# Optimization experiments

Measured on AMD Instinct MI355X. Metric: run time of the kernel, lower is better.

The kernel has to match this reference:

```python
import jax, jax.numpy as jnp
import numpy as np

N_NODES = 100000
N_EDGES = 1000000
D_FEAT = 64
THR_LO, THR_HI = 0.6, 0.8
LOG_CLAMP = -100.0  # torch BCELoss clamps log terms at -100


def setup_inputs() -> dict:
    key = jax.random.key(0)
    k1, k2, k3 = jax.random.split(key, 3)
    edges_nn = jax.random.randint(k1, (N_EDGES, 2), 0, N_NODES, dtype=jnp.int64)
    probas = jax.random.uniform(k2, (N_NODES,), dtype=jnp.float32)
    feats = jax.random.normal(k3, (N_NODES, D_FEAT), dtype=jnp.float32)
    return {"edges_nn": edges_nn, "probas": probas, "feats": feats}


def reference(edges_nn, probas, feats):
    # Per-edge endpoint probabilities. [E]
    pi = probas[edges_nn[:, 0]]
    pj = probas[edges_nn[:, 1]]

    # Similar edges: both endpoints confidently positive (label 1).
    mask_sim = (pi >= THR_HI) & (pj >= THR_HI)
    # Dissimilar edges: one confident positive, the other confident negative (label 0).
    mask_disim = ((pi >= THR_HI) & (pj < THR_LO)) | ((pj >= THR_HI) & (pi < THR_LO))

    # Gather endpoint features and compute pairwise L2 distance for ALL edges
    # (masked afterwards; avoids dynamic shapes, stays jit-friendly). [E, D] -> [E]
    diff = feats[edges_nn[:, 0]] - feats[edges_nn[:, 1]]
    d = jnp.sqrt(jnp.sum(diff * diff, axis=1))
    p = jnp.exp(-d)  # predicted similarity in (0, 1]

    # BCE per edge (torch-style log clamping at -100).
    #   sim   (target 1): -log(p)   = d (clamped)
    #   disim (target 0): -log(1-p)
    bce_sim = -jnp.maximum(jnp.log(p), LOG_CLAMP)
    bce_disim = -jnp.maximum(jnp.log1p(-p), LOG_CLAMP)

    n_sim = jnp.sum(mask_sim).astype(jnp.float32)
    n_disim = jnp.sum(mask_disim).astype(jnp.float32)
    total = n_sim + n_disim

    # Class-balancing weights from the original: sim edges weighted by the
    # fraction of disim edges and vice versa.
    pos_weight = n_disim / total
    neg_weight = n_sim / total

    sim_sum = jnp.sum(jnp.where(mask_sim, bce_sim, 0.0))
    disim_sum = jnp.sum(jnp.where(mask_disim, bce_disim, 0.0))

    loss = (sim_sum * pos_weight + disim_sum * neg_weight) / total
    return loss
```

## Files before the change

### kernel.cpp

```cpp
#include <hip/hip_runtime.h>
#include <math.h>

#define N_EDGES   1000000
#define N_NODES   100000
#define THR_LO    0.6f
#define THR_HI    0.8f
#define LOG_CLAMP -100.0f

#define NBLOCKS   2048
#define BLOCK     256

#define CLS_OFF   0x8000
#define QF_OFF    0x10000

#if defined(__has_builtin)
#if __has_builtin(__builtin_amdgcn_cvt_pk_fp8_f32) && __has_builtin(__builtin_amdgcn_cvt_pk_f32_fp8)
#define HAVE_FP8_CVT 1
#endif
#endif

typedef float v2f __attribute__((ext_vector_type(2)));

__device__ __forceinline__ unsigned f32_to_fp8_sw(float f) {
    unsigned u = __float_as_uint(f);
    unsigned s = (u >> 24) & 0x80u;
    float a = fabsf(f);
    if (a >= 448.f) return s | 0x7Eu;
    unsigned au = u & 0x7FFFFFFFu;
    int E = (int)(au >> 23) - 127;
    if (E >= -6) {
        unsigned m   = au & 0x7FFFFFu;
        unsigned keep = m >> 20;
        unsigned rem  = m & 0xFFFFFu;
        keep += (rem > 0x80000u) || (rem == 0x80000u && (keep & 1u));
        unsigned val = (((unsigned)(E + 7)) << 3) + keep;
        return s | val;
    } else {
        float q = a * 512.0f;
        unsigned k = (unsigned)(q + 0.5f);
        return s | k;
    }
}

__device__ __forceinline__ unsigned pack4_fp8(float4 v) {
#if HAVE_FP8_CVT
    int w = 0;
    w = __builtin_amdgcn_cvt_pk_fp8_f32(v.x, v.y, w, false);
    w = __builtin_amdgcn_cvt_pk_fp8_f32(v.z, v.w, w, true);
    return (unsigned)w;
#else
    return f32_to_fp8_sw(v.x) | (f32_to_fp8_sw(v.y) << 8) |
           (f32_to_fp8_sw(v.z) << 16) | (f32_to_fp8_sw(v.w) << 24);
#endif
}

__device__ __forceinline__ float fp8_to_f32_sw(unsigned byte) {
    unsigned s  = (byte & 0x80u) << 24;
    unsigned em = (byte & 0x7Fu) << 20;
    return __uint_as_float(s | em) * 0x1p+120f;
}

__device__ __forceinline__ float sq8(unsigned a, unsigned b) {
#if HAVE_FP8_CVT
    v2f a0 = __builtin_amdgcn_cvt_pk_f32_fp8((int)a, false);
    v2f a1 = __builtin_amdgcn_cvt_pk_f32_fp8((int)a, true);
    v2f b0 = __builtin_amdgcn_cvt_pk_f32_fp8((int)b, false);
    v2f b1 = __builtin_amdgcn_cvt_pk_f32_fp8((int)b, true);
    float d0 = a0.x - b0.x, d1 = a0.y - b0.y;
    float d2 = a1.x - b1.x, d3 = a1.y - b1.y;
#else
    float d0 = fp8_to_f32_sw(a & 255u)         - fp8_to_f32_sw(b & 255u);
    float d1 = fp8_to_f32_sw((a >> 8) & 255u)  - fp8_to_f32_sw((b >> 8) & 255u);
    float d2 = fp8_to_f32_sw((a >> 16) & 255u) - fp8_to_f32_sw((b >> 16) & 255u);
    float d3 = fp8_to_f32_sw(a >> 24)          - fp8_to_f32_sw(b >> 24);
#endif
    return d0 * d0 + d1 * d1 + d2 * d2 + d3 * d3;
}

__device__ __forceinline__ float sq16(uint4 A, uint4 B) {
    return sq8(A.x, B.x) + sq8(A.y, B.y) + sq8(A.z, B.z) + sq8(A.w, B.w);
}

__device__ __forceinline__ void accum_edge(float s, int simflag,
                                           float& sim, float& dis) {
    float d = sqrtf(s);
    if (simflag) {
        sim += fminf(d, 100.0f);
    } else {
        float p = expf(-d);
        dis += -fmaxf(log1pf(-p), LOG_CLAMP);
    }
}

__global__ void __launch_bounds__(BLOCK)
prep_kernel(const float* __restrict__ probas,
            const float4* __restrict__ feats,
            unsigned* __restrict__ cls,
            unsigned* __restrict__ qf) {
    int t = blockIdx.x * blockDim.x + threadIdx.x;
    const int NF4 = N_NODES * 16;
    if (t < NF4) {
        qf[t] = pack4_fp8(feats[t]);
    }
    if (t < N_NODES / 16) {
        unsigned w = 0;
        #pragma unroll
        for (int k = 0; k < 16; ++k) {
            float p = probas[t * 16 + k];
            unsigned c = (p >= THR_HI ? 1u : 0u) | (p < THR_LO ? 2u : 0u);
            w |= c << (2 * k);
        }
        cls[t] = w;
    }
}

__global__ void __launch_bounds__(BLOCK)
edge_loss_kernel(const int2* __restrict__ edges,
                 const unsigned* __restrict__ cls,
                 const uint4* __restrict__ qfeat,
                 float4* __restrict__ part) {
    const int lane = threadIdx.x & 63;
    const int wave = threadIdx.x >> 6;
    const int grp  = lane >> 2;
    const int sub  = lane & 3;

    __shared__ int sh_i[4][64];
    __shared__ int sh_j[4][64];

    float sim = 0.f, dis = 0.f, ns = 0.f, nd = 0.f;

    const int gstride = gridDim.x * blockDim.x;
    for (int base = blockIdx.x * blockDim.x; base < N_EDGES; base += gstride) {
        int e = base + threadIdx.x;
        bool in = (e < N_EDGES);
        int2 ij = in ? edges[e] : make_int2(0, 0);
        unsigned ci = (cls[ij.x >> 4] >> ((ij.x & 15) * 2)) & 3u;
        unsigned cj = (cls[ij.y >> 4] >> ((ij.y & 15) * 2)) & 3u;
        bool msim = in && ((ci & cj & 1u) != 0u);
        bool mdis = in && ((((ci & 1u) & (cj >> 1)) | ((cj & 1u) & (ci >> 1))) != 0u);

        unsigned long long balsim = __ballot(msim);
        unsigned long long baldis = __ballot(mdis);
        unsigned long long m      = balsim | baldis;
        if (lane == 0) {
            ns += (float)__popcll(balsim);
            nd += (float)__popcll(baldis);
        }
        int count = __popcll(m);

        if (msim | mdis) {
            int prefix = __popcll(m & ((1ULL << lane) - 1ULL));
            sh_i[wave][prefix] = ij.x | (msim ? (int)0x80000000 : 0);
            sh_j[wave][prefix] = ij.y;
        }
        __syncthreads();

        for (int t = grp; t < count; t += 32) {
            bool h2 = (t + 16) < count;
            int  tb = h2 ? t + 16 : t;

            int xa_i = sh_i[wave][t],  xa_j = sh_j[wave][t];
            int xb_i = sh_i[wave][tb], xb_j = sh_j[wave][tb];

            const uint4* rai = qfeat + (size_t)(xa_i & 0x7FFFFFFF) * 4;
            const uint4* raj = qfeat + (size_t)xa_j * 4;
            const uint4* rbi = qfeat + (size_t)(xb_i & 0x7FFFFFFF) * 4;
            const uint4* rbj = qfeat + (size_t)xb_j * 4;

            uint4 A = rai[sub];
            uint4 B = raj[sub];
            uint4 C = rbi[sub];
            uint4 D = rbj[sub];

            float s1 = sq16(A, B);
            float s2 = sq16(C, D);

            s1 += __shfl_xor(s1, 1); s1 += __shfl_xor(s1, 2);
            s2 += __shfl_xor(s2, 1); s2 += __shfl_xor(s2, 2);

            if (sub == 0) {
                accum_edge(s1, ((unsigned)xa_i) >> 31, sim, dis);
                if (h2) accum_edge(s2, ((unsigned)xb_i) >> 31, sim, dis);
            }
        }
        __syncthreads();
    }

    #pragma unroll
    for (int off = 32; off > 0; off >>= 1) {
        sim += __shfl_down(sim, off);
        dis += __shfl_down(dis, off);
        ns  += __shfl_down(ns,  off);
        nd  += __shfl_down(nd,  off);
    }
    __shared__ float lds[4][4];
    if (lane == 0) {
        lds[wave][0] = sim; lds[wave][1] = dis;
        lds[wave][2] = ns;  lds[wave][3] = nd;
    }
    __syncthreads();
    if (threadIdx.x == 0) {
        float a = 0.f, b = 0.f, c = 0.f, d4 = 0.f;
        #pragma unroll
        for (int w = 0; w < 4; ++w) {
            a += lds[w][0]; b += lds[w][1]; c += lds[w][2]; d4 += lds[w][3];
        }
        part[blockIdx.x] = make_float4(a, b, c, d4);
    }
}

__global__ void __launch_bounds__(BLOCK)
finalize_kernel(const float4* __restrict__ part,
                float* __restrict__ out) {
    float a = 0.f, b = 0.f, c = 0.f, d4 = 0.f;
    for (int i = threadIdx.x; i < NBLOCKS; i += BLOCK) {
        float4 p = part[i];
        a += p.x; b += p.y; c += p.z; d4 += p.w;
    }
    #pragma unroll
    for (int off = 32; off > 0; off >>= 1) {
        a  += __shfl_down(a,  off);
        b  += __shfl_down(b,  off);
        c  += __shfl_down(c,  off);
        d4 += __shfl_down(d4, off);
    }
    __shared__ float lds[4][4];
    int lane = threadIdx.x & 63;
    int wave = threadIdx.x >> 6;
    if (lane == 0) {
        lds[wave][0] = a; lds[wave][1] = b; lds[wave][2] = c; lds[wave][3] = d4;
    }
    __syncthreads();
    if (threadIdx.x == 0) {
        float sim_sum = 0.f, disim_sum = 0.f, n_sim = 0.f, n_disim = 0.f;
        #pragma unroll
        for (int w = 0; w < 4; ++w) {
            sim_sum   += lds[w][0];
            disim_sum += lds[w][1];
            n_sim     += lds[w][2];
            n_disim   += lds[w][3];
        }
        float total = n_sim + n_disim;
        out[0] = (sim_sum * (n_disim / total) +
                  disim_sum * (n_sim / total)) / total;
    }
}

extern "C" void kernel_launch(void* const* d_in, const int* in_sizes, int n_in,
                              void* d_out, int out_size, void* d_ws, size_t ws_size,
                              hipStream_t stream) {
    const int*   edges  = (const int*)d_in[0];
    const float* probas = (const float*)d_in[1];
    const float* feats  = (const float*)d_in[2];

    float4*   part = (float4*)d_ws;
    unsigned* cls  = (unsigned*)((char*)d_ws + CLS_OFF);
    unsigned* qf   = (unsigned*)((char*)d_ws + QF_OFF);

    const int NF4 = N_NODES * 16;
    prep_kernel<<<(NF4 + BLOCK - 1) / BLOCK, BLOCK, 0, stream>>>(
        probas, (const float4*)feats, cls, qf);

    edge_loss_kernel<<<NBLOCKS, BLOCK, 0, stream>>>(
        (const int2*)edges, cls, (const uint4*)qf, part);

    finalize_kernel<<<1, BLOCK, 0, stream>>>(part, (float*)d_out);
}
```

Measured before the change: 95.84 us.

## Use one block per 256 edges with block-wide compaction of active edges

Replaces the grid-stride loop over 2048 persistent blocks with one block per 256 edges (about 3907 blocks). Active edges are compacted across the whole block through a per-wave count in shared memory, so all 64 four-lane groups share the compacted work instead of each wave handling only its own survivors. This is meant to improve load balance and remove the per-iteration barriers, at the cost of more blocks, more partial sums for the finalize kernel to reduce, and a larger workspace offset layout.

Result: no change. 95.05 us (median of 2 runs) (-0.8%).

```diff
diff --git a/kernel.cpp b/kernel.cpp
--- a/kernel.cpp
+++ b/kernel.cpp
@@ -7,11 +7,11 @@
 #define THR_HI    0.8f
 #define LOG_CLAMP -100.0f
 
-#define NBLOCKS   2048
 #define BLOCK     256
-
-#define CLS_OFF   0x8000
-#define QF_OFF    0x10000
+#define NBLK      ((N_EDGES + BLOCK - 1) / BLOCK)
+
+#define CLS_OFF   0x10000
+#define QF_OFF    0x18000
 
 #if defined(__has_builtin)
 #if __has_builtin(__builtin_amdgcn_cvt_pk_fp8_f32) && __has_builtin(__builtin_amdgcn_cvt_pk_f32_fp8)
@@ -29,7 +29,7 @@
     unsigned au = u & 0x7FFFFFFFu;
     int E = (int)(au >> 23) - 127;
     if (E >= -6) {
-        unsigned m   = au & 0x7FFFFFu;
+        unsigned m    = au & 0x7FFFFFu;
         unsigned keep = m >> 20;
         unsigned rem  = m & 0xFFFFFu;
         keep += (rem > 0x80000u) || (rem == 0x80000u && (keep & 1u));
@@ -121,69 +121,73 @@
                  float4* __restrict__ part) {
     const int lane = threadIdx.x & 63;
     const int wave = threadIdx.x >> 6;
-    const int grp  = lane >> 2;
-    const int sub  = lane & 3;
-
-    __shared__ int sh_i[4][64];
-    __shared__ int sh_j[4][64];
+    const int g    = threadIdx.x >> 2;
+    const int sub  = threadIdx.x & 3;
+
+    __shared__ int sh_i[BLOCK];
+    __shared__ int sh_j[BLOCK];
+    __shared__ unsigned wcnt[4];
 
     float sim = 0.f, dis = 0.f, ns = 0.f, nd = 0.f;
 
-    const int gstride = gridDim.x * blockDim.x;
-    for (int base = blockIdx.x * blockDim.x; base < N_EDGES; base += gstride) {
-        int e = base + threadIdx.x;
-        bool in = (e < N_EDGES);
-        int2 ij = in ? edges[e] : make_int2(0, 0);
-        unsigned ci = (cls[ij.x >> 4] >> ((ij.x & 15) * 2)) & 3u;
-        unsigned cj = (cls[ij.y >> 4] >> ((ij.y & 15) * 2)) & 3u;
-        bool msim = in && ((ci & cj & 1u) != 0u);
-        bool mdis = in && ((((ci & 1u) & (cj >> 1)) | ((cj & 1u) & (ci >> 1))) != 0u);
-
-        unsigned long long balsim = __ballot(msim);
-        unsigned long long baldis = __ballot(mdis);
-        unsigned long long m      = balsim | baldis;
-        if (lane == 0) {
-            ns += (float)__popcll(balsim);
-            nd += (float)__popcll(baldis);
-        }
-        int count = __popcll(m);
-
-        if (msim | mdis) {
-            int prefix = __popcll(m & ((1ULL << lane) - 1ULL));
-            sh_i[wave][prefix] = ij.x | (msim ? (int)0x80000000 : 0);
-            sh_j[wave][prefix] = ij.y;
-        }
-        __syncthreads();
-
-        for (int t = grp; t < count; t += 32) {
-            bool h2 = (t + 16) < count;
-            int  tb = h2 ? t + 16 : t;
-
-            int xa_i = sh_i[wave][t],  xa_j = sh_j[wave][t];
-            int xb_i = sh_i[wave][tb], xb_j = sh_j[wave][tb];
-
-            const uint4* rai = qfeat + (size_t)(xa_i & 0x7FFFFFFF) * 4;
-            const uint4* raj = qfeat + (size_t)xa_j * 4;
-            const uint4* rbi = qfeat + (size_t)(xb_i & 0x7FFFFFFF) * 4;
-            const uint4* rbj = qfeat + (size_t)xb_j * 4;
-
-            uint4 A = rai[sub];
-            uint4 B = raj[sub];
-            uint4 C = rbi[sub];
-            uint4 D = rbj[sub];
-
-            float s1 = sq16(A, B);
-            float s2 = sq16(C, D);
-
-            s1 += __shfl_xor(s1, 1); s1 += __shfl_xor(s1, 2);
-            s2 += __shfl_xor(s2, 1); s2 += __shfl_xor(s2, 2);
-
-            if (sub == 0) {
-                accum_edge(s1, ((unsigned)xa_i) >> 31, sim, dis);
-                if (h2) accum_edge(s2, ((unsigned)xb_i) >> 31, sim, dis);
-            }
-        }
-        __syncthreads();
+    int e = blockIdx.x * BLOCK + threadIdx.x;
+    bool in = (e < N_EDGES);
+    int2 ij = in ? edges[e] : make_int2(0, 0);
+    unsigned ci = (cls[ij.x >> 4] >> ((ij.x & 15) * 2)) & 3u;
+    unsigned cj = (cls[ij.y >> 4] >> ((ij.y & 15) * 2)) & 3u;
+    bool msim = in && ((ci & cj & 1u) != 0u);
+    bool mdis = in && ((((ci & 1u) & (cj >> 1)) | ((cj & 1u) & (ci >> 1))) != 0u);
+
+    unsigned long long balsim = __ballot(msim);
+    unsigned long long baldis = __ballot(mdis);
+    unsigned long long m      = balsim | baldis;
+    if (lane == 0) {
+        ns = (float)__popcll(balsim);
+        nd = (float)__popcll(baldis);
+        wcnt[wave] = (unsigned)__popcll(m);
+    }
+    __syncthreads();
+
+    unsigned w0 = wcnt[0], w1 = wcnt[1], w2 = wcnt[2], w3 = wcnt[3];
+    int total = (int)(w0 + w1 + w2 + w3);
+    int wbase = (wave > 0 ? (int)w0 : 0) + (wave > 1 ? (int)w1 : 0)
+              + (wave > 2 ? (int)w2 : 0);
+
+    if (msim | mdis) {
+        int prefix = __popcll(m & ((1ULL << lane) - 1ULL));
+        int pos = wbase + prefix;
+        sh_i[pos] = ij.x | (msim ? (int)0x80000000 : 0);
+        sh_j[pos] = ij.y;
+    }
+    __syncthreads();
+
+    for (int t = g; t < total; t += 128) {
+        bool h2 = (t + 64) < total;
+        int  tb = h2 ? t + 64 : t;
+
+        int xa_i = sh_i[t],  xa_j = sh_j[t];
+        int xb_i = sh_i[tb], xb_j = sh_j[tb];
+
+        const uint4* rai = qfeat + (size_t)(xa_i & 0x7FFFFFFF) * 4;
+        const uint4* raj = qfeat + (size_t)xa_j * 4;
+        const uint4* rbi = qfeat + (size_t)(xb_i & 0x7FFFFFFF) * 4;
+        const uint4* rbj = qfeat + (size_t)xb_j * 4;
+
+        uint4 A = rai[sub];
+        uint4 B = raj[sub];
+        uint4 C = rbi[sub];
+        uint4 D = rbj[sub];
+
+        float s1 = sq16(A, B);
+        float s2 = sq16(C, D);
+
+        s1 += __shfl_xor(s1, 1); s1 += __shfl_xor(s1, 2);
+        s2 += __shfl_xor(s2, 1); s2 += __shfl_xor(s2, 2);
+
+        if (sub == 0) {
+            accum_edge(s1, ((unsigned)xa_i) >> 31, sim, dis);
+            if (h2) accum_edge(s2, ((unsigned)xb_i) >> 31, sim, dis);
+        }
     }
 
     #pragma unroll
@@ -213,7 +217,7 @@
 finalize_kernel(const float4* __restrict__ part,
                 float* __restrict__ out) {
     float a = 0.f, b = 0.f, c = 0.f, d4 = 0.f;
-    for (int i = threadIdx.x; i < NBLOCKS; i += BLOCK) {
+    for (int i = threadIdx.x; i < NBLK; i += BLOCK) {
         float4 p = part[i];
         a += p.x; b += p.y; c += p.z; d4 += p.w;
     }
@@ -261,7 +265,7 @@
     prep_kernel<<<(NF4 + BLOCK - 1) / BLOCK, BLOCK, 0, stream>>>(
         probas, (const float4*)feats, cls, qf);
 
-    edge_loss_kernel<<<NBLOCKS, BLOCK, 0, stream>>>(
+    edge_loss_kernel<<<NBLK, BLOCK, 0, stream>>>(
         (const int2*)edges, cls, (const uint4*)qf, part);
 
     finalize_kernel<<<1, BLOCK, 0, stream>>>(part, (float*)d_out);
```
